# Performance work log

Hardware: AMD Instinct MI355X
Metric: run time of the kernel (lower is better)

Reference implementation:

```python
import jax, jax.numpy as jnp
import numpy as np

N_NODES = 100000
N_EDGES = 1600000
N_GRAPHS = 64
D_IN, D_HID, D_OUT = 256, 128, 64
EPS = 1e-5


def gcn_conv(x, edge_index, edge_weight, W, b):
    """PyG GCNConv: add_self_loops=True, normalize=True (sym deg norm), bias."""
    n = x.shape[0]
    row = jnp.concatenate([edge_index[0], jnp.arange(n)])      # source
    col = jnp.concatenate([edge_index[1], jnp.arange(n)])      # target
    w = jnp.concatenate([edge_weight, jnp.ones((n,), x.dtype)])
    deg = jax.ops.segment_sum(w, col, num_segments=n)
    dinv = jnp.where(deg > 0, jax.lax.rsqrt(jnp.maximum(deg, EPS)), 0.0)
    norm = dinv[row] * w * dinv[col]                           # [E+N]
    h = x @ W                                                  # [N, out]
    msg = h[row] * norm[:, None]                               # [E+N, out]
    out = jax.ops.segment_sum(msg, col, num_segments=n)
    return out + b


def layer_norm(x, gamma, beta):
    mu = jnp.mean(x, axis=-1, keepdims=True)
    var = jnp.mean(jnp.square(x - mu), axis=-1, keepdims=True)
    return (x - mu) * jax.lax.rsqrt(var + EPS) * gamma + beta


def setup_inputs() -> dict:
    key = jax.random.key(0)
    ks = jax.random.split(key, 12)
    x = jax.random.normal(ks[0], (N_NODES, D_IN), jnp.float32)
    edge_index = jax.random.randint(ks[1], (2, N_EDGES), 0, N_NODES, jnp.int32)
    edge_weight = jax.random.uniform(ks[2], (N_EDGES,), jnp.float32)
    batch = jnp.sort(jax.random.randint(ks[3], (N_NODES,), 0, N_GRAPHS, jnp.int32))
    s1 = 1.0 / np.sqrt(D_IN)
    s2 = 1.0 / np.sqrt(D_HID)
    return {
        "x": x, "edge_index": edge_index, "edge_weight": edge_weight, "batch": batch,
        "W1": jax.random.uniform(ks[4], (D_IN, D_HID), jnp.float32, -s1, s1),
        "b1": jnp.zeros((D_HID,), jnp.float32),
        "g1": jnp.ones((D_HID,), jnp.float32),
        "bt1": jnp.zeros((D_HID,), jnp.float32),
        "W2": jax.random.uniform(ks[5], (D_HID, D_OUT), jnp.float32, -s2, s2),
        "b2": jnp.zeros((D_OUT,), jnp.float32),
        "g2": jnp.ones((D_OUT,), jnp.float32),
        "bt2": jnp.zeros((D_OUT,), jnp.float32),
    }


def reference(x, edge_index, edge_weight, batch, W1, b1, g1, bt1, W2, b2, g2, bt2):
    # ConvLayer 1: GCNConv -> relu -> LayerNorm(node)
    h = gcn_conv(x, edge_index, edge_weight, W1, b1)
    h = layer_norm(jax.nn.relu(h), g1, bt1)
    # dropout is identity in eval mode
    # ConvLayer 2
    h = gcn_conv(h, edge_index, edge_weight, W2, b2)
    h = layer_norm(jax.nn.relu(h), g2, bt2)
    # global mean pool over batch vector
    sums = jax.ops.segment_sum(h, batch, num_segments=N_GRAPHS)
    cnts = jax.ops.segment_sum(jnp.ones((h.shape[0],), h.dtype), batch, num_segments=N_GRAPHS)
    pooled = sums / jnp.maximum(cnts, 1.0)[:, None]
    return jax.nn.sigmoid(pooled)
```

## Files before the change

### kernel.cpp

```cpp
#include <hip/hip_runtime.h>
#include <cstdint>

#define EPSV 1e-5f

typedef __bf16 bf16x8 __attribute__((ext_vector_type(8)));
typedef __bf16 bf16x2 __attribute__((ext_vector_type(2)));
typedef float  f32x4  __attribute__((ext_vector_type(4)));
typedef unsigned long long u64;

#define DEG_BLOCKS 512

__device__ __forceinline__ unsigned char f32_to_fp8(float x) {
    const int p = __builtin_amdgcn_cvt_pk_fp8_f32(x, x, 0, false);
    return (unsigned char)(p & 0xFF);
}

__global__ __launch_bounds__(256) void k_scanA(const u64* __restrict__ dc,
                                               float* __restrict__ dinv,
                                               int* __restrict__ cnt,
                                               int* __restrict__ bsum, int N) {
    __shared__ int ws[4];
    const int i = blockIdx.x * 256 + threadIdx.x;
    int v = 0;
    if (i < N) {
        const u64 p = dc[i];
        v = (int)(p >> 40);
        const float deg = 1.0f + (float)(p & 0xFFFFFFFFFFull) * (1.0f / 16777216.0f);
        dinv[i] = rsqrtf(deg);
        cnt[i] = v;
    }
#pragma unroll
    for (int o = 32; o >= 1; o >>= 1) v += __shfl_xor(v, o);
    if ((threadIdx.x & 63) == 0) ws[threadIdx.x >> 6] = v;
    __syncthreads();
    if (threadIdx.x == 0) bsum[blockIdx.x] = ws[0] + ws[1] + ws[2] + ws[3];
}

__global__ __launch_bounds__(256) void k_scanB(const int* __restrict__ cnt,
                                               const int* __restrict__ bsum,
                                               int* __restrict__ off, int N) {
    __shared__ int pw[4];
    __shared__ int lw[4];
    __shared__ int sbase;
    const int bid = blockIdx.x;
    const int lane = threadIdx.x & 63, w = threadIdx.x >> 6;

    int pre = 0;
    for (int j = threadIdx.x; j < bid; j += 256) pre += bsum[j];
#pragma unroll
    for (int o = 32; o >= 1; o >>= 1) pre += __shfl_xor(pre, o);
    if (lane == 0) pw[w] = pre;
    __syncthreads();
    if (threadIdx.x == 0) sbase = pw[0] + pw[1] + pw[2] + pw[3];

    const int i = bid * 256 + threadIdx.x;
    const int v = (i < N) ? cnt[i] : 0;
    int s = v;
#pragma unroll
    for (int o = 1; o < 64; o <<= 1) {
        const int t = __shfl_up(s, o);
        if (lane >= o) s += t;
    }
    if (lane == 63) lw[w] = s;
    __syncthreads();
    int add = sbase;
    for (int k = 0; k < w; ++k) add += lw[k];
    if (i < N) off[i] = add + s - v;
}

__global__ __launch_bounds__(256) void k_fill(const int* __restrict__ ei,
                                              const float* __restrict__ ew,
                                              const float* __restrict__ dinv,
                                              const int* __restrict__ off,
                                              const unsigned short* __restrict__ rank,
                                              float2* __restrict__ ern, int E) {
    const int e = blockIdx.x * 256 + threadIdx.x;
    if (e >= E) return;
    const int r = ei[e];
    const int c = ei[E + e];
    const int p = off[c] + (int)rank[e];
    ern[p] = make_float2(__int_as_float(r), dinv[r] * ew[e] * dinv[c]);
}

__global__ __launch_bounds__(256) void k_wcvt(const float* __restrict__ W1,
                                              __bf16* __restrict__ Wt1,
                                              const float* __restrict__ W2,
                                              __bf16* __restrict__ Wt2) {
    const int idx = blockIdx.x * 256 + threadIdx.x;
    if (idx < 256 * 128) {
        const int k = idx >> 7, c = idx & 127;
        Wt1[(((k >> 3) << 7) + c) * 8 + (k & 7)] = (__bf16)W1[idx];
    } else if (idx < 256 * 128 + 128 * 64) {
        const int j = idx - 256 * 128;
        const int k = j >> 6, c = j & 63;
        Wt2[(((k >> 3) << 6) + c) * 8 + (k & 7)] = (__bf16)W2[j];
    }
}

template <int K, int NOUT, bool ABF16>
__device__ __forceinline__ void mm_body(int bid, int tid, const void* __restrict__ Xv,
                                        const __bf16* __restrict__ WtB,
                                        unsigned char* __restrict__ H, int N) {
    constexpr int NCB = NOUT / 16;
    constexpr int NKB = K / 32;
    const int w = tid >> 6, l = tid & 63;
    const int r0 = l & 15, kq = l >> 4;
    const long tb0 = (long)bid * 128 + w * 32;
    const long ar0 = (tb0 + r0) < N ? (tb0 + r0) : (long)N - 1;
    const long ar1 = (tb0 + 16 + r0) < N ? (tb0 + 16 + r0) : (long)N - 1;

    f32x4 acc[2][NCB];
#pragma unroll
    for (int rf = 0; rf < 2; ++rf)
#pragma unroll
        for (int cb = 0; cb < NCB; ++cb) acc[rf][cb] = (f32x4){0.f, 0.f, 0.f, 0.f};

#define LDA(kb, a0, a1)                                                          \
    {                                                                            \
        const int koff = (kb) * 32 + kq * 8;                                     \
        if constexpr (ABF16) {                                                   \
            a0 = *reinterpret_cast<const bf16x8*>((const __bf16*)Xv + ar0 * K + koff); \
            a1 = *reinterpret_cast<const bf16x8*>((const __bf16*)Xv + ar1 * K + koff); \
        } else {                                                                 \
            const float* p0 = (const float*)Xv + ar0 * K + koff;                 \
            const float* p1 = (const float*)Xv + ar1 * K + koff;                 \
            const float4 u0 = *reinterpret_cast<const float4*>(p0);              \
            const float4 u1 = *reinterpret_cast<const float4*>(p0 + 4);          \
            const float4 u2 = *reinterpret_cast<const float4*>(p1);              \
            const float4 u3 = *reinterpret_cast<const float4*>(p1 + 4);          \
            a0[0] = (__bf16)u0.x; a0[1] = (__bf16)u0.y; a0[2] = (__bf16)u0.z;    \
            a0[3] = (__bf16)u0.w; a0[4] = (__bf16)u1.x; a0[5] = (__bf16)u1.y;    \
            a0[6] = (__bf16)u1.z; a0[7] = (__bf16)u1.w;                          \
            a1[0] = (__bf16)u2.x; a1[1] = (__bf16)u2.y; a1[2] = (__bf16)u2.z;    \
            a1[3] = (__bf16)u2.w; a1[4] = (__bf16)u3.x; a1[5] = (__bf16)u3.y;    \
            a1[6] = (__bf16)u3.z; a1[7] = (__bf16)u3.w;                          \
        }                                                                        \
    }

#define LDB(kb, b)                                                               \
    {                                                                            \
        const __bf16* bp = WtB + (long)(((kb) * 4 + kq) * NOUT + r0) * 8;        \
        _Pragma("unroll") for (int cb = 0; cb < NCB; ++cb)                       \
            b[cb] = *reinterpret_cast<const bf16x8*>(bp + cb * 128);             \
    }

    bf16x8 aC0, aC1, aN0, aN1;
    bf16x8 bC[NCB], bN[NCB];
    LDA(0, aC0, aC1);
    LDB(0, bC);
#pragma unroll
    for (int kb = 0; kb < NKB; ++kb) {
        if (kb + 1 < NKB) {
            LDA(kb + 1, aN0, aN1);
            LDB(kb + 1, bN);
        }
#pragma unroll
        for (int cb = 0; cb < NCB; ++cb) {
            acc[0][cb] = __builtin_amdgcn_mfma_f32_16x16x32_bf16(aC0, bC[cb], acc[0][cb], 0, 0, 0);
            acc[1][cb] = __builtin_amdgcn_mfma_f32_16x16x32_bf16(aC1, bC[cb], acc[1][cb], 0, 0, 0);
        }
        aC0 = aN0; aC1 = aN1;
#pragma unroll
        for (int cb = 0; cb < NCB; ++cb) bC[cb] = bN[cb];
    }
#undef LDA
#undef LDB

    const int orow = kq * 4;
#pragma unroll
    for (int rf = 0; rf < 2; ++rf)
#pragma unroll
        for (int cb = 0; cb < NCB; ++cb)
#pragma unroll
            for (int r = 0; r < 4; ++r) {
                const long gr = tb0 + rf * 16 + orow + r;
                if (gr < N) H[gr * NOUT + cb * 16 + r0] = f32_to_fp8(acc[rf][cb][r]);
            }
}

__global__ __launch_bounds__(256) void k_pre(const float* __restrict__ X,
                                             const __bf16* __restrict__ Wt1,
                                             unsigned char* __restrict__ H1, int N, int NBM,
                                             const int* __restrict__ ei,
                                             const float* __restrict__ ew,
                                             u64* __restrict__ dc,
                                             unsigned short* __restrict__ rank, int E) {
    const int bid = blockIdx.x;
    if (bid < DEG_BLOCKS) {
        const int stride = DEG_BLOCKS * 256;
        for (int e = bid * 256 + threadIdx.x; e < E; e += stride) {
            const int c = ei[E + e];
            const u64 pack = (1ull << 40) | (u64)(ew[e] * 16777216.0f);
            const u64 old = atomicAdd(&dc[c], pack);
            rank[e] = (unsigned short)(old >> 40);
        }
    } else {
        mm_body<256, 128, false>(bid - DEG_BLOCKS, threadIdx.x, X, Wt1, H1, N);
    }
}

__global__ __launch_bounds__(256) void k_mm2(const __bf16* __restrict__ X,
                                             const __bf16* __restrict__ Wt2,
                                             unsigned char* __restrict__ H, int N) {
    mm_body<128, 64, true>(blockIdx.x, threadIdx.x, X, Wt2, H, N);
}

__global__ __launch_bounds__(256) void k_gat128(const unsigned char* __restrict__ H,
                                                const int* __restrict__ off,
                                                const int* __restrict__ cnt,
                                                const float2* __restrict__ ern,
                                                const float* __restrict__ dinv,
                                                const float* __restrict__ bias,
                                                const float* __restrict__ gm,
                                                const float* __restrict__ bt,
                                                __bf16* __restrict__ Out, int N) {
    const long wv = ((long)blockIdx.x * 256 + threadIdx.x) >> 6;
    const int lane = threadIdx.x & 63;
    if (wv >= N) return;
    const int s = off[wv];
    const int n = cnt[wv];
    const float d = dinv[wv];
    const unsigned short* Hp = reinterpret_cast<const unsigned short*>(H);

    const unsigned int h0 = Hp[wv * 64 + lane];
    float ax = __builtin_amdgcn_cvt_f32_fp8(h0, 0) * d * d;
    float ay = __builtin_amdgcn_cvt_f32_fp8(h0, 1) * d * d;

    int e = 0;
    for (; e + 8 <= n; e += 8) {
        float2 q[8];
#pragma unroll
        for (int j = 0; j < 8; ++j) q[j] = ern[s + e + j];
        unsigned int u[8];
#pragma unroll
        for (int j = 0; j < 8; ++j)
            u[j] = Hp[(long)__float_as_int(q[j].x) * 64 + lane];
#pragma unroll
        for (int j = 0; j < 8; ++j) {
            ax = fmaf(q[j].y, __builtin_amdgcn_cvt_f32_fp8(u[j], 0), ax);
            ay = fmaf(q[j].y, __builtin_amdgcn_cvt_f32_fp8(u[j], 1), ay);
        }
    }
    for (; e < n; ++e) {
        const float2 q = ern[s + e];
        const unsigned int u = Hp[(long)__float_as_int(q.x) * 64 + lane];
        ax = fmaf(q.y, __builtin_amdgcn_cvt_f32_fp8(u, 0), ax);
        ay = fmaf(q.y, __builtin_amdgcn_cvt_f32_fp8(u, 1), ay);
    }

    const float ux = fmaxf(ax + bias[2 * lane], 0.f);
    const float uy = fmaxf(ay + bias[2 * lane + 1], 0.f);
    float s1 = ux + uy, s2 = ux * ux + uy * uy;
#pragma unroll
    for (int o = 32; o >= 1; o >>= 1) {
        s1 += __shfl_xor(s1, o);
        s2 += __shfl_xor(s2, o);
    }
    const float mu = s1 * (1.f / 128.f);
    const float var = s2 * (1.f / 128.f) - mu * mu;
    const float rs = rsqrtf(var + EPSV);
    bf16x2 ob;
    ob[0] = (__bf16)((ux - mu) * rs * gm[2 * lane] + bt[2 * lane]);
    ob[1] = (__bf16)((uy - mu) * rs * gm[2 * lane + 1] + bt[2 * lane + 1]);
    reinterpret_cast<bf16x2*>(Out)[wv * 64 + lane] = ob;
}

__global__ __launch_bounds__(256) void k_gat64(const unsigned char* __restrict__ H,
                                               const int* __restrict__ off,
                                               const int* __restrict__ cnt,
                                               const float2* __restrict__ ern,
                                               const float* __restrict__ dinv,
                                               const float* __restrict__ bias,
                                               const float* __restrict__ gm,
                                               const float* __restrict__ bt,
                                               float* __restrict__ Out, int N) {
    const long wv = ((long)blockIdx.x * 256 + threadIdx.x) >> 6;
    const int lane = threadIdx.x & 63;
    if (wv >= N) return;
    const int s = off[wv];
    const int n = cnt[wv];
    const float d = dinv[wv];

    float acc = __builtin_amdgcn_cvt_f32_fp8((unsigned int)H[wv * 64 + lane], 0) * d * d;
    int e = 0;
    for (; e + 8 <= n; e += 8) {
        float2 q[8];
#pragma unroll
        for (int j = 0; j < 8; ++j) q[j] = ern[s + e + j];
        unsigned int u[8];
#pragma unroll
        for (int j = 0; j < 8; ++j)
            u[j] = H[(long)__float_as_int(q[j].x) * 64 + lane];
#pragma unroll
        for (int j = 0; j < 8; ++j)
            acc = fmaf(q[j].y, __builtin_amdgcn_cvt_f32_fp8(u[j], 0), acc);
    }
    for (; e < n; ++e) {
        const float2 q = ern[s + e];
        const unsigned int u = H[(long)__float_as_int(q.x) * 64 + lane];
        acc = fmaf(q.y, __builtin_amdgcn_cvt_f32_fp8(u, 0), acc);
    }

    const float u = fmaxf(acc + bias[lane], 0.f);
    float s1 = u, s2 = u * u;
#pragma unroll
    for (int o = 32; o >= 1; o >>= 1) {
        s1 += __shfl_xor(s1, o);
        s2 += __shfl_xor(s2, o);
    }
    const float mu = s1 * (1.f / 64.f);
    const float var = s2 * (1.f / 64.f) - mu * mu;
    const float rs = rsqrtf(var + EPSV);
    Out[wv * 64 + lane] = (u - mu) * rs * gm[lane] + bt[lane];
}

__global__ __launch_bounds__(256) void k_pool(const float* __restrict__ C,
                                              const int* __restrict__ batch,
                                              float* __restrict__ pool,
                                              int N, int chunk) {
    const int wg = blockIdx.x * 4 + (threadIdx.x >> 6);
    const int lane = threadIdx.x & 63;
    long i = (long)wg * chunk;
    const long end = (i + chunk < (long)N) ? i + chunk : (long)N;
    if (i >= end) return;

    int cur = batch[i];
    float acc = 0.f;
    int cn = 0;
    while (i < end) {
        if (i + 8 <= end && batch[i + 7] == cur) {
            float v[8];
#pragma unroll
            for (int j = 0; j < 8; ++j) v[j] = C[(i + j) * 64 + lane];
            acc += ((v[0] + v[1]) + (v[2] + v[3])) + ((v[4] + v[5]) + (v[6] + v[7]));
            cn += 8;
            i += 8;
            continue;
        }
        const int b = batch[i];
        if (b != cur) {
            unsafeAtomicAdd(&pool[cur * 64 + lane], acc);
            if (lane == 0) unsafeAtomicAdd(&pool[64 * 64 + cur], (float)cn);
            cur = b;
            acc = 0.f;
            cn = 0;
        }
        acc += C[i * 64 + lane];
        ++cn;
        ++i;
    }
    unsafeAtomicAdd(&pool[cur * 64 + lane], acc);
    if (lane == 0) unsafeAtomicAdd(&pool[64 * 64 + cur], (float)cn);
}

__global__ __launch_bounds__(256) void k_final(const float* __restrict__ pool,
                                               float* __restrict__ out) {
    const int i = blockIdx.x * 256 + threadIdx.x;
    if (i < 4096) {
        const int g = i >> 6;
        const float cnt = fmaxf(pool[64 * 64 + g], 1.0f);
        const float v = pool[i] / cnt;
        out[i] = 1.f / (1.f + expf(-v));
    }
}

extern "C" void kernel_launch(void* const* d_in, const int* in_sizes, int n_in,
                              void* d_out, int out_size, void* d_ws, size_t ws_size,
                              hipStream_t stream) {
    const float* x   = (const float*)d_in[0];
    const int*   ei  = (const int*)d_in[1];
    const float* ew  = (const float*)d_in[2];
    const int*   bat = (const int*)d_in[3];
    const float* W1  = (const float*)d_in[4];
    const float* b1  = (const float*)d_in[5];
    const float* g1  = (const float*)d_in[6];
    const float* bt1 = (const float*)d_in[7];
    const float* W2  = (const float*)d_in[8];
    const float* b2  = (const float*)d_in[9];
    const float* g2  = (const float*)d_in[10];
    const float* bt2 = (const float*)d_in[11];
    const int N = in_sizes[3];
    const int E = in_sizes[2];
    const int NB = (N + 255) / 256;

    u64*    dc   = (u64*)d_ws;
    float*  pool = (float*)(dc + N);
    float2* ern  = (float2*)(pool + 64 * 64 + 64);
    unsigned char* Ah = (unsigned char*)(ern + E);
    __bf16* Bh   = (__bf16*)(Ah + (long)N * 128);
    float*  Cf   = (float*)(Bh + (long)N * 128);
    float*  dinv = Cf + (long)N * 64;
    int*    cnt  = (int*)(dinv + N);
    int*    off  = cnt + N;
    int*    bsum = off + N;
    unsigned short* rank = (unsigned short*)(bsum + ((NB + 3) & ~3));
    __bf16* Wt1  = (__bf16*)(rank + E);
    __bf16* Wt2  = Wt1 + 128 * 256;

    const int nbE = (E + 255) / 256;
    const int nbW = (int)(((long)N * 64 + 255) / 256);
    const int NBM = (N + 127) / 128;

    hipMemsetAsync(dc, 0, (size_t)N * 8 + (64 * 64 + 64) * 4, stream);
    k_wcvt<<<(256 * 128 + 128 * 64 + 255) / 256, 256, 0, stream>>>(W1, Wt1, W2, Wt2);

    k_pre<<<DEG_BLOCKS + NBM, 256, 0, stream>>>(x, Wt1, Ah, N, NBM, ei, ew, dc, rank, E);

    k_scanA<<<NB, 256, 0, stream>>>(dc, dinv, cnt, bsum, N);
    k_scanB<<<NB, 256, 0, stream>>>(cnt, bsum, off, N);
    k_fill<<<nbE, 256, 0, stream>>>(ei, ew, dinv, off, rank, ern, E);

    k_gat128<<<nbW, 256, 0, stream>>>(Ah, off, cnt, ern, dinv, b1, g1, bt1, Bh, N);

    k_mm2<<<NBM, 256, 0, stream>>>(Bh, Wt2, Ah, N);
    k_gat64<<<nbW, 256, 0, stream>>>(Ah, off, cnt, ern, dinv, b2, g2, bt2, Cf, N);

    const int chunk = (N + 1023) / 1024;
    k_pool<<<256, 256, 0, stream>>>(Cf, bat, pool, N, chunk);
    k_final<<<16, 256, 0, stream>>>(pool, (float*)d_out);
}
```

Before: 314.5 us.

## Move CSR fill into the first GEMM launch, pad degree atomics, store layer-2 output as bf16

Degree accumulation becomes its own launch, and its per-node counters are padded to 128-byte spacing to reduce atomic contention on shared cache lines. The CSR edge fill now runs alongside the first matmul blocks in one fused launch, in place of the degree atomics. The layer-2 output buffer is stored as bf16, which halves the traffic into the pooling kernel at some precision cost. The padding makes the zero-fill memset 16x larger, and the degree atomics no longer overlap with the GEMM.

```diff
diff --git a/kernel.cpp b/kernel.cpp
--- a/kernel.cpp
+++ b/kernel.cpp
@@ -8,11 +8,25 @@
 typedef float  f32x4  __attribute__((ext_vector_type(4)));
 typedef unsigned long long u64;
 
-#define DEG_BLOCKS 512
+#define FILL_BLOCKS 512
 
 __device__ __forceinline__ unsigned char f32_to_fp8(float x) {
     const int p = __builtin_amdgcn_cvt_pk_fp8_f32(x, x, 0, false);
     return (unsigned char)(p & 0xFF);
+}
+
+__global__ __launch_bounds__(256) void k_degacc(const int* __restrict__ ei,
+                                                const float* __restrict__ ew,
+                                                u64* __restrict__ dc,
+                                                unsigned short* __restrict__ rank,
+                                                int E) {
+    const int e = blockIdx.x * 256 + threadIdx.x;
+    if (e < E) {
+        const int c = ei[E + e];
+        const u64 pack = (1ull << 40) | (u64)(ew[e] * 16777216.0f);
+        const u64 old = atomicAdd(&dc[(long)c << 4], pack);
+        rank[e] = (unsigned short)(old >> 40);
+    }
 }
 
 __global__ __launch_bounds__(256) void k_scanA(const u64* __restrict__ dc,
@@ -23,7 +37,7 @@
     const int i = blockIdx.x * 256 + threadIdx.x;
     int v = 0;
     if (i < N) {
-        const u64 p = dc[i];
+        const u64 p = dc[(long)i << 4];
         v = (int)(p >> 40);
         const float deg = 1.0f + (float)(p & 0xFFFFFFFFFFull) * (1.0f / 16777216.0f);
         dinv[i] = rsqrtf(deg);
@@ -66,20 +80,6 @@
     int add = sbase;
     for (int k = 0; k < w; ++k) add += lw[k];
     if (i < N) off[i] = add + s - v;
-}
-
-__global__ __launch_bounds__(256) void k_fill(const int* __restrict__ ei,
-                                              const float* __restrict__ ew,
-                                              const float* __restrict__ dinv,
-                                              const int* __restrict__ off,
-                                              const unsigned short* __restrict__ rank,
-                                              float2* __restrict__ ern, int E) {
-    const int e = blockIdx.x * 256 + threadIdx.x;
-    if (e >= E) return;
-    const int r = ei[e];
-    const int c = ei[E + e];
-    const int p = off[c] + (int)rank[e];
-    ern[p] = make_float2(__int_as_float(r), dinv[r] * ew[e] * dinv[c]);
 }
 
 __global__ __launch_bounds__(256) void k_wcvt(const float* __restrict__ W1,
@@ -178,24 +178,26 @@
             }
 }
 
-__global__ __launch_bounds__(256) void k_pre(const float* __restrict__ X,
-                                             const __bf16* __restrict__ Wt1,
-                                             unsigned char* __restrict__ H1, int N, int NBM,
-                                             const int* __restrict__ ei,
-                                             const float* __restrict__ ew,
-                                             u64* __restrict__ dc,
-                                             unsigned short* __restrict__ rank, int E) {
+__global__ __launch_bounds__(256) void k_fuse(const int* __restrict__ ei,
+                                              const float* __restrict__ ew,
+                                              const float* __restrict__ dinv,
+                                              const int* __restrict__ off,
+                                              const unsigned short* __restrict__ rank,
+                                              float2* __restrict__ ern, int E,
+                                              const float* __restrict__ X,
+                                              const __bf16* __restrict__ Wt1,
+                                              unsigned char* __restrict__ H1, int N) {
     const int bid = blockIdx.x;
-    if (bid < DEG_BLOCKS) {
-        const int stride = DEG_BLOCKS * 256;
+    if (bid < FILL_BLOCKS) {
+        const int stride = FILL_BLOCKS * 256;
         for (int e = bid * 256 + threadIdx.x; e < E; e += stride) {
+            const int r = ei[e];
             const int c = ei[E + e];
-            const u64 pack = (1ull << 40) | (u64)(ew[e] * 16777216.0f);
-            const u64 old = atomicAdd(&dc[c], pack);
-            rank[e] = (unsigned short)(old >> 40);
+            const int p = off[c] + (int)rank[e];
+            ern[p] = make_float2(__int_as_float(r), dinv[r] * ew[e] * dinv[c]);
         }
     } else {
-        mm_body<256, 128, false>(bid - DEG_BLOCKS, threadIdx.x, X, Wt1, H1, N);
+        mm_body<256, 128, false>(bid - FILL_BLOCKS, threadIdx.x, X, Wt1, H1, N);
     }
 }
 
@@ -273,7 +275,7 @@
                                                const float* __restrict__ bias,
                                                const float* __restrict__ gm,
                                                const float* __restrict__ bt,
-                                               float* __restrict__ Out, int N) {
+                                               __bf16* __restrict__ Out, int N) {
     const long wv = ((long)blockIdx.x * 256 + threadIdx.x) >> 6;
     const int lane = threadIdx.x & 63;
     if (wv >= N) return;
@@ -311,10 +313,10 @@
     const float mu = s1 * (1.f / 64.f);
     const float var = s2 * (1.f / 64.f) - mu * mu;
     const float rs = rsqrtf(var + EPSV);
-    Out[wv * 64 + lane] = (u - mu) * rs * gm[lane] + bt[lane];
-}
-
-__global__ __launch_bounds__(256) void k_pool(const float* __restrict__ C,
+    Out[wv * 64 + lane] = (__bf16)((u - mu) * rs * gm[lane] + bt[lane]);
+}
+
+__global__ __launch_bounds__(256) void k_pool(const __bf16* __restrict__ C,
                                               const int* __restrict__ batch,
                                               float* __restrict__ pool,
                                               int N, int chunk) {
@@ -331,7 +333,7 @@
         if (i + 8 <= end && batch[i + 7] == cur) {
             float v[8];
 #pragma unroll
-            for (int j = 0; j < 8; ++j) v[j] = C[(i + j) * 64 + lane];
+            for (int j = 0; j < 8; ++j) v[j] = (float)C[(i + j) * 64 + lane];
             acc += ((v[0] + v[1]) + (v[2] + v[3])) + ((v[4] + v[5]) + (v[6] + v[7]));
             cn += 8;
             i += 8;
@@ -345,7 +347,7 @@
             acc = 0.f;
             cn = 0;
         }
-        acc += C[i * 64 + lane];
+        acc += (float)C[i * 64 + lane];
         ++cn;
         ++i;
     }
@@ -384,12 +386,12 @@
     const int NB = (N + 255) / 256;
 
     u64*    dc   = (u64*)d_ws;
-    float*  pool = (float*)(dc + N);
+    float*  pool = (float*)(dc + (long)N * 16);
     float2* ern  = (float2*)(pool + 64 * 64 + 64);
     unsigned char* Ah = (unsigned char*)(ern + E);
     __bf16* Bh   = (__bf16*)(Ah + (long)N * 128);
-    float*  Cf   = (float*)(Bh + (long)N * 128);
-    float*  dinv = Cf + (long)N * 64;
+    __bf16* Cb   = Bh + (long)N * 128;
+    float*  dinv = (float*)(Cb + (long)N * 64);
     int*    cnt  = (int*)(dinv + N);
     int*    off  = cnt + N;
     int*    bsum = off + N;
@@ -401,21 +403,22 @@
     const int nbW = (int)(((long)N * 64 + 255) / 256);
     const int NBM = (N + 127) / 128;
 
-    hipMemsetAsync(dc, 0, (size_t)N * 8 + (64 * 64 + 64) * 4, stream);
+    hipMemsetAsync(dc, 0, (size_t)N * 16 * 8 + (64 * 64 + 64) * 4, stream);
     k_wcvt<<<(256 * 128 + 128 * 64 + 255) / 256, 256, 0, stream>>>(W1, Wt1, W2, Wt2);
 
-    k_pre<<<DEG_BLOCKS + NBM, 256, 0, stream>>>(x, Wt1, Ah, N, NBM, ei, ew, dc, rank, E);
-
+    k_degacc<<<nbE, 256, 0, stream>>>(ei, ew, dc, rank, E);
     k_scanA<<<NB, 256, 0, stream>>>(dc, dinv, cnt, bsum, N);
     k_scanB<<<NB, 256, 0, stream>>>(cnt, bsum, off, N);
-    k_fill<<<nbE, 256, 0, stream>>>(ei, ew, dinv, off, rank, ern, E);
+
+    k_fuse<<<FILL_BLOCKS + NBM, 256, 0, stream>>>(ei, ew, dinv, off, rank, ern, E,
+                                                  x, Wt1, Ah, N);
 
     k_gat128<<<nbW, 256, 0, stream>>>(Ah, off, cnt, ern, dinv, b1, g1, bt1, Bh, N);
 
     k_mm2<<<NBM, 256, 0, stream>>>(Bh, Wt2, Ah, N);
-    k_gat64<<<nbW, 256, 0, stream>>>(Ah, off, cnt, ern, dinv, b2, g2, bt2, Cf, N);
+    k_gat64<<<nbW, 256, 0, stream>>>(Ah, off, cnt, ern, dinv, b2, g2, bt2, Cb, N);
 
     const int chunk = (N + 1023) / 1024;
-    k_pool<<<256, 256, 0, stream>>>(Cf, bat, pool, N, chunk);
+    k_pool<<<256, 256, 0, stream>>>(Cb, bat, pool, N, chunk);
     k_final<<<16, 256, 0, stream>>>(pool, (float*)d_out);
 }
```

Measured after the change: 322.4 us. 2.5% more time.
